# Kernel tuning notes

Measured on AMD Instinct MI355X. Metric: run time of the kernel, lower is better.

The kernel has to match this reference:

```python
import jax, jax.numpy as jnp
import numpy as np

N, T, C, H = 512, 64, 64, 4
HD = C // H
FE = 4  # forward_expansion
EPS = 1e-5


def _p(key, shape, scale=0.05):
    return jax.random.normal(key, shape, dtype=jnp.float32) * scale


def setup_inputs() -> dict:
    key = jax.random.key(0)
    ks = jax.random.split(key, 24)
    return {
        'value': jax.random.normal(ks[0], (N, T, C), dtype=jnp.float32),
        'key_t': jax.random.normal(ks[1], (N, T, C), dtype=jnp.float32),
        'query': jax.random.normal(ks[2], (N, T, C), dtype=jnp.float32),
        'adj': jax.random.uniform(ks[3], (N, N), dtype=jnp.float32),
        # SSelfAttention params (nn.Linear weights, applied as x @ W.T)
        'Wv': _p(ks[4], (HD, HD)), 'Wk': _p(ks[5], (HD, HD)), 'Wq': _p(ks[6], (HD, HD)),
        'Wo': _p(ks[7], (C, C)), 'bo': jnp.zeros((C,), jnp.float32),
        # LayerNorms
        'g1': jnp.ones((C,), jnp.float32), 'b1': jnp.zeros((C,), jnp.float32),
        'g2': jnp.ones((C,), jnp.float32), 'b2': jnp.zeros((C,), jnp.float32),
        # FFN
        'Wf1': _p(ks[8], (FE * C, C)), 'bf1': jnp.zeros((FE * C,), jnp.float32),
        'Wf2': _p(ks[9], (C, FE * C)), 'bf2': jnp.zeros((C,), jnp.float32),
        # GCN (two GraphConvolution layers: adj @ (x @ W) + b, ReLU between)
        'Wg1': _p(ks[10], (C, C)), 'bg1': jnp.zeros((C,), jnp.float32),
        'Wg2': _p(ks[11], (C, C)), 'bg2': jnp.zeros((C,), jnp.float32),
        # gating linears
        'Wo1': _p(ks[12], (C, C)), 'bo1': jnp.zeros((C,), jnp.float32),
        'Wo2': _p(ks[13], (C, C)), 'bo2': jnp.zeros((C,), jnp.float32),
    }


def _layernorm(x, g, b):
    m = jnp.mean(x, axis=-1, keepdims=True)
    v = jnp.mean((x - m) ** 2, axis=-1, keepdims=True)
    return (x - m) * jax.lax.rsqrt(v + EPS) * g + b


def reference(value, key_t, query, adj, Wv, Wk, Wq, Wo, bo, g1, b1, g2, b2,
              Wf1, bf1, Wf2, bf2, Wg1, bg1, Wg2, bg2, Wo1, bo1, Wo2, bo2):
    n, t, c = query.shape
    # --- SSelfAttention: attention across nodes (q/k axes are nodes) ---
    vh = value.reshape(n, t, H, HD) @ Wv.T
    kh = key_t.reshape(n, t, H, HD) @ Wk.T
    qh = query.reshape(n, t, H, HD) @ Wq.T
    energy = jnp.einsum('qthd,kthd->qkth', qh, kh)  # [N,N,T,H]
    att = jax.nn.softmax(energy / jnp.sqrt(jnp.float32(c)), axis=1)
    attn_out = jnp.einsum('qkth,kthd->qthd', att, vh).reshape(n, t, c)
    attn_out = attn_out @ Wo.T + bo
    # --- residual + norm + FFN + norm (dropout = identity, eval mode) ---
    x = _layernorm(attn_out + query, g1, b1)
    ffn = jax.nn.relu(x @ Wf1.T + bf1) @ Wf2.T + bf2
    out1 = _layernorm(ffn + x, g2, b2)
    # --- InstanceNorm2d(1) on adj: normalize over whole NxN map (no affine) ---
    am = jnp.mean(adj)
    av = jnp.mean((adj - am) ** 2)
    adj_n = (adj - am) * jax.lax.rsqrt(av + EPS)
    # --- GCN applied per-timestep, vectorized over T ---
    h = jax.nn.relu(jnp.einsum('nm,mtc->ntc', adj_n, query @ Wg1.T) + bg1)
    out2 = jnp.einsum('nm,mtc->ntc', adj_n, h @ Wg2.T) + bg2
    # --- gated fusion ---
    g = jax.nn.sigmoid(out1 @ Wo1.T + bo1 + out2 @ Wo2.T + bo2)
    return g * out1 + (1.0 - g) * out2
```

## Files before the change

kernel.cpp:

```cpp
#include <hip/hip_runtime.h>

#define LN_EPS 1e-5f

typedef __attribute__((ext_vector_type(4))) short short4v;
typedef __attribute__((ext_vector_type(4))) float float4v;

__device__ __forceinline__ float wave_sum(float v) {
#pragma unroll
  for (int o = 32; o > 0; o >>= 1) v += __shfl_xor(v, o, 64);
  return v;
}

__device__ __forceinline__ unsigned short f2b(float f) {
  unsigned int u = __float_as_uint(f);
  u += 0x7fffu + ((u >> 16) & 1u);
  return (unsigned short)(u >> 16);
}

__device__ __forceinline__ float b2f(unsigned short h) {
  return __uint_as_float(((unsigned int)h) << 16);
}

__device__ __forceinline__ float4v mfma_16x16x16_bf16(short4v a, short4v b,
                                                      float4v c) {
#if __has_builtin(__builtin_amdgcn_mfma_f32_16x16x16bf16_1k)
  return __builtin_amdgcn_mfma_f32_16x16x16bf16_1k(a, b, c, 0, 0, 0);
#else
  float4v d;
  asm volatile(
      "v_mfma_f32_16x16x16_bf16 %0, %1, %2, %3\n\ts_nop 7\n\ts_nop 7"
      : "=v"(d)
      : "v"(a), "v"(b), "v"(c));
  return d;
#endif
}

__global__ __launch_bounds__(256) void adj_part(const float* __restrict__ adj,
                                                float* __restrict__ ps,
                                                float* __restrict__ pss) {
  __shared__ float r1[4], r2[4];
  const int b = blockIdx.x, tid = threadIdx.x;
  float v0 = adj[b * 512 + tid], v1 = adj[b * 512 + 256 + tid];
  float s = v0 + v1;
  float ss = fmaf(v0, v0, v1 * v1);
  s = wave_sum(s);
  ss = wave_sum(ss);
  if ((tid & 63) == 0) { r1[tid >> 6] = s; r2[tid >> 6] = ss; }
  __syncthreads();
  if (tid == 0) {
    ps[b] = r1[0] + r1[1] + r1[2] + r1[3];
    pss[b] = r2[0] + r2[1] + r2[2] + r2[3];
  }
}

__global__ __launch_bounds__(256) void prep_kernel(
    const float* __restrict__ adj, const float* __restrict__ ps,
    const float* __restrict__ pss, const float* __restrict__ query,
    const float* __restrict__ Wg1, const float* __restrict__ Wf1,
    const float* __restrict__ Wf2, const float* __restrict__ Wo1,
    const float* __restrict__ Wo2, const float* __restrict__ Wg2,
    const float* __restrict__ bg2, const float* __restrict__ bo1,
    const float* __restrict__ bo2, unsigned short* __restrict__ anh,
    unsigned short* __restrict__ anl, unsigned short* __restrict__ Yfh,
    unsigned short* __restrict__ Yfl, unsigned short* __restrict__ Wf1f,
    unsigned short* __restrict__ Wf2f, unsigned short* __restrict__ Wo1f,
    unsigned short* __restrict__ Wg2hf, unsigned short* __restrict__ Wg2lf,
    unsigned short* __restrict__ W32hf, unsigned short* __restrict__ W32lf,
    float* __restrict__ c2) {
  __shared__ float r1[4], r2[4];
  __shared__ __align__(16) float pool[8320];
  const int tid = threadIdx.x, b = blockIdx.x;
  if (b < 256) {
    float s = ps[tid] + ps[tid + 256];
    float ss = pss[tid] + pss[tid + 256];
    s = wave_sum(s);
    ss = wave_sum(ss);
    if ((tid & 63) == 0) { r1[tid >> 6] = s; r2[tid >> 6] = ss; }
    __syncthreads();
    const float sum = r1[0] + r1[1] + r1[2] + r1[3];
    const float sqs = r2[0] + r2[1] + r2[2] + r2[3];
    const float am = sum * (1.f / 262144.f);
    const float var = sqs * (1.f / 262144.f) - am * am;
    const float rs = rsqrtf(var + LN_EPS);
    const int i = (b * 256 + tid) * 4;
    float4 v = *(const float4*)&adj[i];
    float vals[4] = {(v.x - am) * rs, (v.y - am) * rs, (v.z - am) * rs,
                     (v.w - am) * rs};
    unsigned short th[4], tl[4];
#pragma unroll
    for (int j = 0; j < 4; ++j) {
      th[j] = f2b(vals[j]);
      tl[j] = f2b(vals[j] - b2f(th[j]));
    }
    *(short4v*)&anh[i] = *(short4v*)th;
    *(short4v*)&anl[i] = *(short4v*)tl;
  } else if (b < 320) {
    const int id = (b - 256) * 256 + tid;
    const int n = id >> 6, k = id & 63;
    Wf1f[((k >> 4) * 256 + n) * 16 + (k & 15)] = f2b(Wf1[id]);
  } else if (b < 384) {
    const int id = (b - 320) * 256 + tid;
    const int n = id >> 8, k = id & 255;
    Wf2f[((k >> 4) * 64 + n) * 16 + (k & 15)] = f2b(Wf2[id]);
  } else if (b < 896) {
    const int pb = b - 384;
    const int w = tid >> 6, lane = tid & 63;
    const int mt = pb & 31;
    const int t = (pb >> 5) * 4 + w;
    float* xs = pool;
    float* Ls = pool + 256;
    float wc[64];
#pragma unroll
    for (int e = 0; e < 16; ++e)
      *(float4*)&wc[e * 4] = *(const float4*)&Wg1[lane * 64 + e * 4];
#pragma unroll 4
    for (int ms = 0; ms < 16; ++ms) {
      const int r = (mt * 16 + ms) * 64 + t;
      xs[w * 64 + lane] = query[r * 64 + lane];
      float acc = 0.f;
#pragma unroll
      for (int e = 0; e < 64; ++e) acc = fmaf(xs[w * 64 + e], wc[e], acc);
      Ls[(w * 16 + ms) * 68 + lane] = acc;
    }
    unsigned int dh[8], dl[8];
#pragma unroll
    for (int j = 0; j < 8; ++j) {
      float v0 = Ls[(w * 16 + 2 * j) * 68 + lane];
      float v1 = Ls[(w * 16 + 2 * j + 1) * 68 + lane];
      unsigned int h0 = f2b(v0), h1 = f2b(v1);
      unsigned int l0 = f2b(v0 - b2f((unsigned short)h0));
      unsigned int l1 = f2b(v1 - b2f((unsigned short)h1));
      dh[j] = h0 | (h1 << 16);
      dl[j] = l0 | (l1 << 16);
    }
    const int off = ((mt * 4096) + t * 64 + lane) * 16;
    *(uint4*)(Yfh + off) = *(uint4*)&dh[0];
    *(uint4*)(Yfh + off + 8) = *(uint4*)&dh[4];
    *(uint4*)(Yfl + off) = *(uint4*)&dl[0];
    *(uint4*)(Yfl + off + 8) = *(uint4*)&dl[4];
  } else if (b == 896) {
    for (int i = tid; i < 4096; i += 256) {
      const int n = i >> 6, k = i & 63;
      Wo1f[((k >> 4) * 64 + n) * 16 + (k & 15)] = f2b(Wo1[i]);
    }
  } else if (b == 897) {
    for (int i = tid; i < 4096; i += 256) {
      const int n = i >> 6, k = i & 63;
      const float v = Wg2[i];
      const unsigned short h = f2b(v);
      const unsigned short l = f2b(v - b2f(h));
      Wg2hf[((k >> 4) * 64 + n) * 16 + (k & 15)] = h;
      Wg2lf[((k >> 4) * 64 + n) * 16 + (k & 15)] = l;
    }
  } else {
    float* wo2s = pool;
    float* wg2s = pool + 4096;
    float* bg2s = pool + 8192;
    for (int i = tid; i < 4096; i += 256) {
      wo2s[i] = Wo2[i];
      wg2s[i] = Wg2[i];
    }
    if (tid < 64) bg2s[tid] = bg2[tid];
    __syncthreads();
#pragma unroll 4
    for (int t = 0; t < 16; ++t) {
      const int i = t * 256 + tid;
      const int r = i >> 6, c = i & 63;
      float acc = 0.f;
#pragma unroll
      for (int e = 0; e < 64; ++e)
        acc = fmaf(wo2s[r * 64 + e], wg2s[e * 64 + c], acc);
      const unsigned short h = f2b(acc);
      const unsigned short l = f2b(acc - b2f(h));
      W32hf[((c >> 4) * 64 + r) * 16 + (c & 15)] = h;
      W32lf[((c >> 4) * 64 + r) * 16 + (c & 15)] = l;
    }
    if (tid < 64) {
      float acc = bo1[tid] + bo2[tid];
#pragma unroll
      for (int e = 0; e < 64; ++e)
        acc = fmaf(wo2s[tid * 64 + e], bg2s[e], acc);
      c2[tid] = acc;
    }
  }
}

__global__ __launch_bounds__(512) void qkv2_kernel(
    const float* __restrict__ value, const float* __restrict__ keyt,
    const float* __restrict__ query, const float* __restrict__ Wv,
    const float* __restrict__ Wk, const float* __restrict__ Wq,
    unsigned short* __restrict__ vt, unsigned short* __restrict__ kh,
    unsigned short* __restrict__ qh) {
  __shared__ __align__(16) float wv[256], wk[256], wq[256];
  const int tid = threadIdx.x;
  if (tid < 256) {
    wv[tid] = Wv[tid];
    wk[tid] = Wk[tid];
    wq[tid] = Wq[tid] * 0.125f;
  }
  __syncthreads();
  const int th = blockIdx.x;
  const int t = th >> 2, h = th & 3;
  const int n = tid;
  const int base = t * 64 + h * 16;

  float y[16];
  unsigned short tmp[16];

#define XFORM(SRC, WARR)                                            \
  {                                                                 \
    const float4* p = (const float4*)(SRC + n * 4096 + base);       \
    float x[16];                                                    \
    *(float4*)(x + 0) = p[0];                                       \
    *(float4*)(x + 4) = p[1];                                       \
    *(float4*)(x + 8) = p[2];                                       \
    *(float4*)(x + 12) = p[3];                                      \
    _Pragma("unroll") for (int d = 0; d < 16; ++d) {                \
      float acc = 0.f;                                              \
      _Pragma("unroll") for (int e4 = 0; e4 < 4; ++e4) {            \
        float4 w4 = *(const float4*)&WARR[d * 16 + e4 * 4];         \
        acc = fmaf(w4.x, x[e4 * 4 + 0], acc);                       \
        acc = fmaf(w4.y, x[e4 * 4 + 1], acc);                       \
        acc = fmaf(w4.z, x[e4 * 4 + 2], acc);                       \
        acc = fmaf(w4.w, x[e4 * 4 + 3], acc);                       \
      }                                                             \
      y[d] = acc;                                                   \
    }                                                               \
  }

  XFORM(value, wv)
#pragma unroll
  for (int d = 0; d < 16; ++d) vt[th * 8192 + d * 512 + n] = f2b(y[d]);

  XFORM(keyt, wk)
#pragma unroll
  for (int d = 0; d < 16; ++d) tmp[d] = f2b(y[d]);
  *(int4*)&kh[(th * 512 + n) * 16] = *(int4*)&tmp[0];
  *(int4*)&kh[(th * 512 + n) * 16 + 8] = *(int4*)&tmp[8];

  XFORM(query, wq)
#pragma unroll
  for (int d = 0; d < 16; ++d) tmp[d] = f2b(y[d]);
  *(int4*)&qh[(th * 512 + n) * 16] = *(int4*)&tmp[0];
  *(int4*)&qh[(th * 512 + n) * 16 + 8] = *(int4*)&tmp[8];
#undef XFORM
}

#define VPAD 536
__global__ __launch_bounds__(256) void attn_mfma(
    const unsigned short* __restrict__ qh, const unsigned short* __restrict__ kh,
    const unsigned short* __restrict__ vt, float* __restrict__ o) {
  __shared__ __align__(16) unsigned short Vs[16 * VPAD];
  const int th = blockIdx.x >> 2;
  const int tid = threadIdx.x;
  {
    const unsigned short* vb = vt + th * 8192;
#pragma unroll
    for (int it = 0; it < 4; ++it) {
      const int flat = (it * 256 + tid) * 8;
      const int d = flat >> 9, k = flat & 511;
      *(int4*)&Vs[d * VPAD + k] = *(const int4*)&vb[flat];
    }
  }
  __syncthreads();

  const int lane = tid & 15;
  const int quad = (tid >> 4) & 3;
  const int w = tid >> 6;
  const int q0 = (blockIdx.x & 3) * 128 + w * 32;

  const unsigned short* qbase = qh + th * 8192;
  const unsigned short* kbase = kh + th * 8192;
  short4v qf[2];
#pragma unroll
  for (int ct = 0; ct < 2; ++ct)
    qf[ct] = *(const short4v*)&qbase[(q0 + ct * 16 + lane) * 16 + quad * 4];

  float4v acc[2];
  float l[2];
#pragma unroll
  for (int ct = 0; ct < 2; ++ct) {
    acc[ct].x = 0.f; acc[ct].y = 0.f; acc[ct].z = 0.f; acc[ct].w = 0.f;
    l[ct] = 0.f;
  }
  float4v zero;
  zero.x = 0.f; zero.y = 0.f; zero.z = 0.f; zero.w = 0.f;

  const unsigned short* vrow = &Vs[lane * VPAD];

  for (int kt = 0; kt < 32; ++kt) {
    const short4v kf =
        *(const short4v*)&kbase[(kt * 16 + lane) * 16 + quad * 4];
    const short4v vf = *(const short4v*)&vrow[kt * 16 + quad * 4];
#pragma unroll
    for (int ct = 0; ct < 2; ++ct) {
      float4v s = mfma_16x16x16_bf16(kf, qf[ct], zero);
      float p0 = __expf(s.x);
      float p1 = __expf(s.y);
      float p2 = __expf(s.z);
      float p3 = __expf(s.w);
      l[ct] += (p0 + p1) + (p2 + p3);
      unsigned int u0 = __float_as_uint(p0) + 0x8000u;
      unsigned int u1 = __float_as_uint(p1) + 0x8000u;
      unsigned int u2 = __float_as_uint(p2) + 0x8000u;
      unsigned int u3 = __float_as_uint(p3) + 0x8000u;
      union {
        uint2 u;
        short4v s4;
      } pk;
      pk.u.x = __builtin_amdgcn_perm(u1, u0, 0x07060302u);
      pk.u.y = __builtin_amdgcn_perm(u3, u2, 0x07060302u);
      acc[ct] = mfma_16x16x16_bf16(vf, pk.s4, acc[ct]);
    }
  }

#pragma unroll
  for (int ct = 0; ct < 2; ++ct) {
    float lt = l[ct];
    lt += __shfl_xor(lt, 16, 64);
    lt += __shfl_xor(lt, 32, 64);
    const float inv = 1.f / lt;
    float4 out;
    out.x = acc[ct].x * inv;
    out.y = acc[ct].y * inv;
    out.z = acc[ct].z * inv;
    out.w = acc[ct].w * inv;
    const int q = q0 + ct * 16 + lane;
    *(float4*)&o[th * 8192 + q * 16 + quad * 4] = out;
  }
}

__global__ __launch_bounds__(256) void xffn_fused(
    const float* __restrict__ o, const float* __restrict__ query,
    const float* __restrict__ Wo, const float* __restrict__ bo,
    const float* __restrict__ g1, const float* __restrict__ b1,
    const unsigned short* __restrict__ Wf1f, const float* __restrict__ bf1,
    const unsigned short* __restrict__ Wf2f, const float* __restrict__ bf2,
    const float* __restrict__ g2, const float* __restrict__ b2,
    float* __restrict__ out1, unsigned short* __restrict__ out1b) {
  __shared__ float xs_res[64][68];
  __shared__ __align__(16) unsigned short xb[64 * 68];
  __shared__ __align__(16) unsigned short hid[64 * 260];
  __shared__ float bcast[4][64];
  const int tid = threadIdx.x;
  const int w = tid >> 6, lane = tid & 63;
  const int ln = lane & 15, quad = lane >> 4;
  const int n = blockIdx.x;

  {
    float wc[64];
#pragma unroll
    for (int e = 0; e < 16; ++e)
      *(float4*)&wc[e * 4] = *(const float4*)&Wo[lane * 64 + e * 4];
    const float boc = bo[lane], gc = g1[lane], bc1 = b1[lane];
    const int hsel = lane >> 4, dsel = lane & 15;
    for (int i = 0; i < 16; ++i) {
      const int tt = w * 16 + i;
      bcast[w][lane] = o[(tt * 4 + hsel) * 8192 + n * 16 + dsel];
      float acc = 0.f;
#pragma unroll
      for (int e = 0; e < 64; ++e) acc = fmaf(bcast[w][e], wc[e], acc);
      float y = acc + boc + query[(n * 64 + tt) * 64 + lane];
      float mean = wave_sum(y) * 0.015625f;
      float d = y - mean;
      float var = wave_sum(d * d) * 0.015625f;
      float v = d * rsqrtf(var + LN_EPS) * gc + bc1;
      xs_res[tt][lane] = v;
      xb[tt * 68 + lane] = f2b(v);
    }
  }
  __syncthreads();

  {
    const int wm = (w & 1) * 32, wn = (w >> 1) * 128;
    float4v acc[2][8];
#pragma unroll
    for (int i = 0; i < 2; ++i)
#pragma unroll
      for (int j = 0; j < 8; ++j) {
        acc[i][j].x = 0.f; acc[i][j].y = 0.f;
        acc[i][j].z = 0.f; acc[i][j].w = 0.f;
      }
#pragma unroll
    for (int kt = 0; kt < 4; ++kt) {
      short4v a0 = *(const short4v*)&xb[(wm + ln) * 68 + kt * 16 + quad * 4];
      short4v a1 =
          *(const short4v*)&xb[(wm + 16 + ln) * 68 + kt * 16 + quad * 4];
#pragma unroll
      for (int j = 0; j < 8; ++j) {
        short4v bfr = *(const short4v*)&Wf1f[(kt * 256 + wn + j * 16 + ln) * 16 +
                                             quad * 4];
        acc[0][j] = mfma_16x16x16_bf16(a0, bfr, acc[0][j]);
        acc[1][j] = mfma_16x16x16_bf16(a1, bfr, acc[1][j]);
      }
    }
#pragma unroll
    for (int mt = 0; mt < 2; ++mt)
#pragma unroll
      for (int j = 0; j < 8; ++j) {
        const int col = wn + j * 16 + ln;
        const float bb = bf1[col];
#pragma unroll
        for (int reg = 0; reg < 4; ++reg) {
          const int row = wm + mt * 16 + quad * 4 + reg;
          hid[row * 260 + col] = f2b(fmaxf(acc[mt][j][reg] + bb, 0.f));
        }
      }
  }
  __syncthreads();

  {
    float4v acc[4];
#pragma unroll
    for (int j = 0; j < 4; ++j) {
      acc[j].x = 0.f; acc[j].y = 0.f; acc[j].z = 0.f; acc[j].w = 0.f;
    }
#pragma unroll 4
    for (int kt = 0; kt < 16; ++kt) {
      short4v a =
          *(const short4v*)&hid[(w * 16 + ln) * 260 + kt * 16 + quad * 4];
#pragma unroll
      for (int j = 0; j < 4; ++j) {
        short4v bfr =
            *(const short4v*)&Wf2f[(kt * 64 + j * 16 + ln) * 16 + quad * 4];
        acc[j] = mfma_16x16x16_bf16(a, bfr, acc[j]);
      }
    }
#pragma unroll
    for (int reg = 0; reg < 4; ++reg) {
      const int row = w * 16 + quad * 4 + reg;
      float v[4];
      float s = 0.f;
#pragma unroll
      for (int j = 0; j < 4; ++j) {
        v[j] = acc[j][reg] + bf2[j * 16 + ln] + xs_res[row][j * 16 + ln];
        s += v[j];
      }
      s += __shfl_xor(s, 1, 64);
      s += __shfl_xor(s, 2, 64);
      s += __shfl_xor(s, 4, 64);
      s += __shfl_xor(s, 8, 64);
      const float mean = s * 0.015625f;
      float vv = 0.f;
#pragma unroll
      for (int j = 0; j < 4; ++j) {
        const float dd = v[j] - mean;
        vv += dd * dd;
      }
      vv += __shfl_xor(vv, 1, 64);
      vv += __shfl_xor(vv, 2, 64);
      vv += __shfl_xor(vv, 4, 64);
      vv += __shfl_xor(vv, 8, 64);
      const float rs = rsqrtf(vv * 0.015625f + LN_EPS);
#pragma unroll
      for (int j = 0; j < 4; ++j) {
        const float ov = (v[j] - mean) * rs * g2[j * 16 + ln] + b2[j * 16 + ln];
        const int idx = (n * 64 + row) * 64 + j * 16 + ln;
        out1[idx] = ov;
        out1b[idx] = f2b(ov);
      }
    }
  }
}

__global__ __launch_bounds__(256) void gcn_gemm1(
    const unsigned short* __restrict__ Ah, const unsigned short* __restrict__ Al,
    const unsigned short* __restrict__ Bh, const unsigned short* __restrict__ Bl,
    const float* __restrict__ bg1, unsigned short* __restrict__ Hh,
    unsigned short* __restrict__ Hl) {
  const int tid = threadIdx.x;
  const int wave = tid >> 6, lane = tid & 63;
  const int ln = lane & 15, quad = lane >> 4;
  const int wm = (wave & 1) * 32, wn = (wave >> 1) * 64;
  const int m0 = blockIdx.y * 64 + wm;
  const int n0 = blockIdx.x * 128 + wn;

  const unsigned short* ah0 = Ah + (m0 + ln) * 512 + quad * 4;
  const unsigned short* al0 = Al + (m0 + ln) * 512 + quad * 4;
  const unsigned short* bh0 = Bh + (n0 + ln) * 16 + quad * 4;
  const unsigned short* bl0 = Bl + (n0 + ln) * 16 + quad * 4;

  float4v acc[2][4];
#pragma unroll
  for (int i = 0; i < 2; ++i)
#pragma unroll
    for (int j = 0; j < 4; ++j) {
      acc[i][j].x = 0.f; acc[i][j].y = 0.f;
      acc[i][j].z = 0.f; acc[i][j].w = 0.f;
    }

#pragma unroll 2
  for (int kt = 0; kt < 32; ++kt) {
    short4v a0h = *(const short4v*)(ah0 + kt * 16);
    short4v a1h = *(const short4v*)(ah0 + 16 * 512 + kt * 16);
    short4v a0l = *(const short4v*)(al0 + kt * 16);
    short4v a1l = *(const short4v*)(al0 + 16 * 512 + kt * 16);
#pragma unroll
    for (int j = 0; j < 4; ++j) {
      const int boff = (kt * 4096 + j * 16) * 16;
      short4v bh = *(const short4v*)(bh0 + boff);
      short4v bl = *(const short4v*)(bl0 + boff);
      acc[0][j] = mfma_16x16x16_bf16(a0l, bh, acc[0][j]);
      acc[0][j] = mfma_16x16x16_bf16(a0h, bl, acc[0][j]);
      acc[0][j] = mfma_16x16x16_bf16(a0h, bh, acc[0][j]);
      acc[1][j] = mfma_16x16x16_bf16(a1l, bh, acc[1][j]);
      acc[1][j] = mfma_16x16x16_bf16(a1h, bl, acc[1][j]);
      acc[1][j] = mfma_16x16x16_bf16(a1h, bh, acc[1][j]);
    }
  }

#pragma unroll
  for (int mt = 0; mt < 2; ++mt) {
    const int mtile = (m0 + mt * 16) >> 4;
#pragma unroll
    for (int j = 0; j < 4; ++j) {
      const int col = n0 + j * 16 + ln;
      const float bb = bg1[col & 63];
      unsigned short hh[4], hl[4];
#pragma unroll
      for (int reg = 0; reg < 4; ++reg) {
        float v = fmaxf(acc[mt][j][reg] + bb, 0.f);
        hh[reg] = f2b(v);
        hl[reg] = f2b(v - b2f(hh[reg]));
      }
      const int off = (mtile * 4096 + col) * 16 + quad * 4;
      *(uint2*)&Hh[off] = *(uint2*)hh;
      *(uint2*)&Hl[off] = *(uint2*)hl;
    }
  }
}

__global__ __launch_bounds__(256) void gcn_gemm2(
    const unsigned short* __restrict__ Ah, const unsigned short* __restrict__ Al,
    const unsigned short* __restrict__ Bh, const unsigned short* __restrict__ Bl,
    unsigned short* __restrict__ G2h, unsigned short* __restrict__ G2l) {
  const int tid = threadIdx.x;
  const int wave = tid >> 6, lane = tid & 63;
  const int ln = lane & 15, quad = lane >> 4;
  const int wm = (wave & 1) * 32, wn = (wave >> 1) * 64;
  const int m0 = blockIdx.y * 64 + wm;
  const int n0 = blockIdx.x * 128 + wn;

  const unsigned short* ah0 = Ah + (m0 + ln) * 512 + quad * 4;
  const unsigned short* al0 = Al + (m0 + ln) * 512 + quad * 4;
  const unsigned short* bh0 = Bh + (n0 + ln) * 16 + quad * 4;
  const unsigned short* bl0 = Bl + (n0 + ln) * 16 + quad * 4;

  float4v acc[2][4];
#pragma unroll
  for (int i = 0; i < 2; ++i)
#pragma unroll
    for (int j = 0; j < 4; ++j) {
      acc[i][j].x = 0.f; acc[i][j].y = 0.f;
      acc[i][j].z = 0.f; acc[i][j].w = 0.f;
    }

#pragma unroll 2
  for (int kt = 0; kt < 32; ++kt) {
    short4v a0h = *(const short4v*)(ah0 + kt * 16);
    short4v a1h = *(const short4v*)(ah0 + 16 * 512 + kt * 16);
    short4v a0l = *(const short4v*)(al0 + kt * 16);
    short4v a1l = *(const short4v*)(al0 + 16 * 512 + kt * 16);
#pragma unroll
    for (int j = 0; j < 4; ++j) {
      const int boff = (kt * 4096 + j * 16) * 16;
      short4v bh = *(const short4v*)(bh0 + boff);
      short4v bl = *(const short4v*)(bl0 + boff);
      acc[0][j] = mfma_16x16x16_bf16(a0l, bh, acc[0][j]);
      acc[0][j] = mfma_16x16x16_bf16(a0h, bl, acc[0][j]);
      acc[0][j] = mfma_16x16x16_bf16(a0h, bh, acc[0][j]);
      acc[1][j] = mfma_16x16x16_bf16(a1l, bh, acc[1][j]);
      acc[1][j] = mfma_16x16x16_bf16(a1h, bl, acc[1][j]);
      acc[1][j] = mfma_16x16x16_bf16(a1h, bh, acc[1][j]);
    }
  }

#pragma unroll
  for (int mt = 0; mt < 2; ++mt)
#pragma unroll
    for (int j = 0; j < 4; ++j) {
      const int col = n0 + j * 16 + ln;
#pragma unroll
      for (int reg = 0; reg < 4; ++reg) {
        const int row = m0 + mt * 16 + quad * 4 + reg;
        const float v = acc[mt][j][reg];
        const unsigned short h = f2b(v);
        G2h[row * 4096 + col] = h;
        G2l[row * 4096 + col] = f2b(v - b2f(h));
      }
    }
}

__global__ __launch_bounds__(256) void gate_mfma(
    const unsigned short* __restrict__ out1b, const float* __restrict__ out1,
    const unsigned short* __restrict__ G2h, const unsigned short* __restrict__ G2l,
    const unsigned short* __restrict__ Wo1f, const unsigned short* __restrict__ Wg2hf,
    const unsigned short* __restrict__ Wg2lf, const unsigned short* __restrict__ W32hf,
    const unsigned short* __restrict__ W32lf, const float* __restrict__ bg2,
    const float* __restrict__ c2, float* __restrict__ dst) {
  const int tid = threadIdx.x;
  const int wave = tid >> 6, lane = tid & 63;
  const int ln = lane & 15, quad = lane >> 4;
  const int m0 = blockIdx.x * 64 + wave * 16;

  const unsigned short* o1p = out1b + (m0 + ln) * 64 + quad * 4;
  const unsigned short* ghp = G2h + (m0 + ln) * 64 + quad * 4;
  const unsigned short* glp = G2l + (m0 + ln) * 64 + quad * 4;

  float4v aco[4], aca[4];
#pragma unroll
  for (int j = 0; j < 4; ++j) {
    aco[j].x = 0.f; aco[j].y = 0.f; aco[j].z = 0.f; aco[j].w = 0.f;
    aca[j].x = 0.f; aca[j].y = 0.f; aca[j].z = 0.f; aca[j].w = 0.f;
  }

#pragma unroll
  for (int kt = 0; kt < 4; ++kt) {
    const short4v ao = *(const short4v*)(o1p + kt * 16);
    const short4v gh = *(const short4v*)(ghp + kt * 16);
    const short4v gl = *(const short4v*)(glp + kt * 16);
#pragma unroll
    for (int j = 0; j < 4; ++j) {
      const int boff = (kt * 64 + j * 16 + ln) * 16 + quad * 4;
      const short4v wgh = *(const short4v*)(Wg2hf + boff);
      const short4v wgl = *(const short4v*)(Wg2lf + boff);
      const short4v wo1 = *(const short4v*)(Wo1f + boff);
      const short4v w3h = *(const short4v*)(W32hf + boff);
      const short4v w3l = *(const short4v*)(W32lf + boff);
      aco[j] = mfma_16x16x16_bf16(gl, wgh, aco[j]);
      aco[j] = mfma_16x16x16_bf16(gh, wgl, aco[j]);
      aco[j] = mfma_16x16x16_bf16(gh, wgh, aco[j]);
      aca[j] = mfma_16x16x16_bf16(ao, wo1, aca[j]);
      aca[j] = mfma_16x16x16_bf16(gl, w3h, aca[j]);
      aca[j] = mfma_16x16x16_bf16(gh, w3l, aca[j]);
      aca[j] = mfma_16x16x16_bf16(gh, w3h, aca[j]);
    }
  }

#pragma unroll
  for (int j = 0; j < 4; ++j) {
    const int col = j * 16 + ln;
    const float bg2v = bg2[col];
    const float c2v = c2[col];
#pragma unroll
    for (int reg = 0; reg < 4; ++reg) {
      const int row = m0 + quad * 4 + reg;
      const float o2 = aco[j][reg] + bg2v;
      const float a = aca[j][reg] + c2v;
      const float o1v = out1[row * 64 + col];
      const float g = 1.f / (1.f + __expf(-a));
      dst[row * 64 + col] = o2 + g * (o1v - o2);
    }
  }
}

extern "C" void kernel_launch(void* const* d_in, const int* in_sizes, int n_in,
                              void* d_out, int out_size, void* d_ws,
                              size_t ws_size, hipStream_t stream) {
  const float* value = (const float*)d_in[0];
  const float* key_t = (const float*)d_in[1];
  const float* query = (const float*)d_in[2];
  const float* adj = (const float*)d_in[3];
  const float* Wv = (const float*)d_in[4];
  const float* Wk = (const float*)d_in[5];
  const float* Wq = (const float*)d_in[6];
  const float* Wo = (const float*)d_in[7];
  const float* bo = (const float*)d_in[8];
  const float* g1 = (const float*)d_in[9];
  const float* b1 = (const float*)d_in[10];
  const float* g2 = (const float*)d_in[11];
  const float* b2 = (const float*)d_in[12];
  const float* Wf1 = (const float*)d_in[13];
  const float* bf1 = (const float*)d_in[14];
  const float* Wf2 = (const float*)d_in[15];
  const float* bf2 = (const float*)d_in[16];
  const float* Wg1 = (const float*)d_in[17];
  const float* bg1 = (const float*)d_in[18];
  const float* Wg2 = (const float*)d_in[19];
  const float* bg2 = (const float*)d_in[20];
  const float* Wo1 = (const float*)d_in[21];
  const float* bo1 = (const float*)d_in[22];
  const float* Wo2 = (const float*)d_in[23];
  const float* bo2 = (const float*)d_in[24];

  float* ws = (float*)d_ws;
  const size_t M1 = 1048576;
  float* o = ws + 0;
  float* out1 = ws + 2 * M1;
  unsigned short* out1b = (unsigned short*)(ws + 4 * M1);
  unsigned short* qh = (unsigned short*)(ws + 5 * M1);
  unsigned short* kh = (unsigned short*)(ws + 6 * M1);
  unsigned short* vt = (unsigned short*)(ws + 7 * M1);
  unsigned short* Yfh = (unsigned short*)(ws + 8 * M1);
  unsigned short* Yfl = (unsigned short*)(ws + 9 * M1);
  unsigned short* Hrfh = (unsigned short*)(ws + 10 * M1);
  unsigned short* Hrfl = (unsigned short*)(ws + 11 * M1);
  unsigned short* G2h = (unsigned short*)(ws + 12 * M1);
  unsigned short* G2l = (unsigned short*)(ws + 13 * M1);
  unsigned short* anh = (unsigned short*)(ws + 14 * M1);
  unsigned short* anl = (unsigned short*)(ws + 14 * M1 + 131072);
  float* wbase = ws + 14 * M1 + 262144;
  unsigned short* Wf1f = (unsigned short*)(wbase);
  unsigned short* Wf2f = (unsigned short*)(wbase + 8192);
  unsigned short* Wo1f = (unsigned short*)(wbase + 16384);
  unsigned short* Wg2hf = (unsigned short*)(wbase + 18432);
  unsigned short* Wg2lf = (unsigned short*)(wbase + 20480);
  unsigned short* W32hf = (unsigned short*)(wbase + 22528);
  unsigned short* W32lf = (unsigned short*)(wbase + 24576);
  float* c2 = wbase + 26624;
  float* ps = wbase + 26688;
  float* pss = ps + 512;
  float* dst = (float*)d_out;

  adj_part<<<512, 256, 0, stream>>>(adj, ps, pss);
  prep_kernel<<<899, 256, 0, stream>>>(adj, ps, pss, query, Wg1, Wf1, Wf2,
                                       Wo1, Wo2, Wg2, bg2, bo1, bo2, anh, anl,
                                       Yfh, Yfl, Wf1f, Wf2f, Wo1f, Wg2hf,
                                       Wg2lf, W32hf, W32lf, c2);
  qkv2_kernel<<<256, 512, 0, stream>>>(value, key_t, query, Wv, Wk, Wq, vt, kh, qh);
  attn_mfma<<<1024, 256, 0, stream>>>(qh, kh, vt, o);
  xffn_fused<<<512, 256, 0, stream>>>(o, query, Wo, bo, g1, b1, Wf1f, bf1,
                                      Wf2f, bf2, g2, b2, out1, out1b);
  gcn_gemm1<<<dim3(32, 8), 256, 0, stream>>>(anh, anl, Yfh, Yfl, bg1, Hrfh,
                                             Hrfl);
  gcn_gemm2<<<dim3(32, 8), 256, 0, stream>>>(anh, anl, Hrfh, Hrfl, G2h, G2l);
  gate_mfma<<<512, 256, 0, stream>>>(out1b, out1, G2h, G2l, Wo1f, Wg2hf,
                                     Wg2lf, W32hf, W32lf, bg2, c2, dst);
}
```

Baseline: 268.5 us.

## Merge independent stages into fewer launches via block-index dispatch

Merges the eight kernel launches into five. Each new kernel branches on block index so that independent work runs side by side: adj partial sums with the QKV projection, prep work with attention, and the FFN with GCN gemm1. The second GCN gemm is retiled to 64x64 blocks, giving 512 blocks instead of 256 for more parallelism. This removes launch gaps and lets small stages fill idle compute units, at the cost of larger shared memory per block and mixed block types with different register needs.

```diff
diff --git a/kernel.cpp b/kernel.cpp
--- a/kernel.cpp
+++ b/kernel.cpp
@@ -35,177 +35,38 @@
 #endif
 }
 
-__global__ __launch_bounds__(256) void adj_part(const float* __restrict__ adj,
-                                                float* __restrict__ ps,
-                                                float* __restrict__ pss) {
+__global__ __launch_bounds__(256) void s1_kernel(
+    const float* __restrict__ adj, float* __restrict__ ps,
+    float* __restrict__ pss, const float* __restrict__ value,
+    const float* __restrict__ keyt, const float* __restrict__ query,
+    const float* __restrict__ Wv, const float* __restrict__ Wk,
+    const float* __restrict__ Wq, unsigned short* __restrict__ vt,
+    unsigned short* __restrict__ kh, unsigned short* __restrict__ qh) {
   __shared__ float r1[4], r2[4];
+  __shared__ __align__(16) float wv[256], wk[256], wq[256];
   const int b = blockIdx.x, tid = threadIdx.x;
-  float v0 = adj[b * 512 + tid], v1 = adj[b * 512 + 256 + tid];
-  float s = v0 + v1;
-  float ss = fmaf(v0, v0, v1 * v1);
-  s = wave_sum(s);
-  ss = wave_sum(ss);
-  if ((tid & 63) == 0) { r1[tid >> 6] = s; r2[tid >> 6] = ss; }
-  __syncthreads();
-  if (tid == 0) {
-    ps[b] = r1[0] + r1[1] + r1[2] + r1[3];
-    pss[b] = r2[0] + r2[1] + r2[2] + r2[3];
-  }
-}
-
-__global__ __launch_bounds__(256) void prep_kernel(
-    const float* __restrict__ adj, const float* __restrict__ ps,
-    const float* __restrict__ pss, const float* __restrict__ query,
-    const float* __restrict__ Wg1, const float* __restrict__ Wf1,
-    const float* __restrict__ Wf2, const float* __restrict__ Wo1,
-    const float* __restrict__ Wo2, const float* __restrict__ Wg2,
-    const float* __restrict__ bg2, const float* __restrict__ bo1,
-    const float* __restrict__ bo2, unsigned short* __restrict__ anh,
-    unsigned short* __restrict__ anl, unsigned short* __restrict__ Yfh,
-    unsigned short* __restrict__ Yfl, unsigned short* __restrict__ Wf1f,
-    unsigned short* __restrict__ Wf2f, unsigned short* __restrict__ Wo1f,
-    unsigned short* __restrict__ Wg2hf, unsigned short* __restrict__ Wg2lf,
-    unsigned short* __restrict__ W32hf, unsigned short* __restrict__ W32lf,
-    float* __restrict__ c2) {
-  __shared__ float r1[4], r2[4];
-  __shared__ __align__(16) float pool[8320];
-  const int tid = threadIdx.x, b = blockIdx.x;
-  if (b < 256) {
-    float s = ps[tid] + ps[tid + 256];
-    float ss = pss[tid] + pss[tid + 256];
+  if (b < 512) {
+    float v0 = adj[b * 512 + tid], v1 = adj[b * 512 + 256 + tid];
+    float s = v0 + v1;
+    float ss = fmaf(v0, v0, v1 * v1);
     s = wave_sum(s);
     ss = wave_sum(ss);
     if ((tid & 63) == 0) { r1[tid >> 6] = s; r2[tid >> 6] = ss; }
     __syncthreads();
-    const float sum = r1[0] + r1[1] + r1[2] + r1[3];
-    const float sqs = r2[0] + r2[1] + r2[2] + r2[3];
-    const float am = sum * (1.f / 262144.f);
-    const float var = sqs * (1.f / 262144.f) - am * am;
-    const float rs = rsqrtf(var + LN_EPS);
-    const int i = (b * 256 + tid) * 4;
-    float4 v = *(const float4*)&adj[i];
-    float vals[4] = {(v.x - am) * rs, (v.y - am) * rs, (v.z - am) * rs,
-                     (v.w - am) * rs};
-    unsigned short th[4], tl[4];
-#pragma unroll
-    for (int j = 0; j < 4; ++j) {
-      th[j] = f2b(vals[j]);
-      tl[j] = f2b(vals[j] - b2f(th[j]));
-    }
-    *(short4v*)&anh[i] = *(short4v*)th;
-    *(short4v*)&anl[i] = *(short4v*)tl;
-  } else if (b < 320) {
-    const int id = (b - 256) * 256 + tid;
-    const int n = id >> 6, k = id & 63;
-    Wf1f[((k >> 4) * 256 + n) * 16 + (k & 15)] = f2b(Wf1[id]);
-  } else if (b < 384) {
-    const int id = (b - 320) * 256 + tid;
-    const int n = id >> 8, k = id & 255;
-    Wf2f[((k >> 4) * 64 + n) * 16 + (k & 15)] = f2b(Wf2[id]);
-  } else if (b < 896) {
-    const int pb = b - 384;
-    const int w = tid >> 6, lane = tid & 63;
-    const int mt = pb & 31;
-    const int t = (pb >> 5) * 4 + w;
-    float* xs = pool;
-    float* Ls = pool + 256;
-    float wc[64];
-#pragma unroll
-    for (int e = 0; e < 16; ++e)
-      *(float4*)&wc[e * 4] = *(const float4*)&Wg1[lane * 64 + e * 4];
-#pragma unroll 4
-    for (int ms = 0; ms < 16; ++ms) {
-      const int r = (mt * 16 + ms) * 64 + t;
-      xs[w * 64 + lane] = query[r * 64 + lane];
-      float acc = 0.f;
-#pragma unroll
-      for (int e = 0; e < 64; ++e) acc = fmaf(xs[w * 64 + e], wc[e], acc);
-      Ls[(w * 16 + ms) * 68 + lane] = acc;
-    }
-    unsigned int dh[8], dl[8];
-#pragma unroll
-    for (int j = 0; j < 8; ++j) {
-      float v0 = Ls[(w * 16 + 2 * j) * 68 + lane];
-      float v1 = Ls[(w * 16 + 2 * j + 1) * 68 + lane];
-      unsigned int h0 = f2b(v0), h1 = f2b(v1);
-      unsigned int l0 = f2b(v0 - b2f((unsigned short)h0));
-      unsigned int l1 = f2b(v1 - b2f((unsigned short)h1));
-      dh[j] = h0 | (h1 << 16);
-      dl[j] = l0 | (l1 << 16);
-    }
-    const int off = ((mt * 4096) + t * 64 + lane) * 16;
-    *(uint4*)(Yfh + off) = *(uint4*)&dh[0];
-    *(uint4*)(Yfh + off + 8) = *(uint4*)&dh[4];
-    *(uint4*)(Yfl + off) = *(uint4*)&dl[0];
-    *(uint4*)(Yfl + off + 8) = *(uint4*)&dl[4];
-  } else if (b == 896) {
-    for (int i = tid; i < 4096; i += 256) {
-      const int n = i >> 6, k = i & 63;
-      Wo1f[((k >> 4) * 64 + n) * 16 + (k & 15)] = f2b(Wo1[i]);
-    }
-  } else if (b == 897) {
-    for (int i = tid; i < 4096; i += 256) {
-      const int n = i >> 6, k = i & 63;
-      const float v = Wg2[i];
-      const unsigned short h = f2b(v);
-      const unsigned short l = f2b(v - b2f(h));
-      Wg2hf[((k >> 4) * 64 + n) * 16 + (k & 15)] = h;
-      Wg2lf[((k >> 4) * 64 + n) * 16 + (k & 15)] = l;
+    if (tid == 0) {
+      ps[b] = r1[0] + r1[1] + r1[2] + r1[3];
+      pss[b] = r2[0] + r2[1] + r2[2] + r2[3];
     }
   } else {
-    float* wo2s = pool;
-    float* wg2s = pool + 4096;
-    float* bg2s = pool + 8192;
-    for (int i = tid; i < 4096; i += 256) {
-      wo2s[i] = Wo2[i];
-      wg2s[i] = Wg2[i];
-    }
-    if (tid < 64) bg2s[tid] = bg2[tid];
-    __syncthreads();
-#pragma unroll 4
-    for (int t = 0; t < 16; ++t) {
-      const int i = t * 256 + tid;
-      const int r = i >> 6, c = i & 63;
-      float acc = 0.f;
-#pragma unroll
-      for (int e = 0; e < 64; ++e)
-        acc = fmaf(wo2s[r * 64 + e], wg2s[e * 64 + c], acc);
-      const unsigned short h = f2b(acc);
-      const unsigned short l = f2b(acc - b2f(h));
-      W32hf[((c >> 4) * 64 + r) * 16 + (c & 15)] = h;
-      W32lf[((c >> 4) * 64 + r) * 16 + (c & 15)] = l;
-    }
-    if (tid < 64) {
-      float acc = bo1[tid] + bo2[tid];
-#pragma unroll
-      for (int e = 0; e < 64; ++e)
-        acc = fmaf(wo2s[tid * 64 + e], bg2s[e], acc);
-      c2[tid] = acc;
-    }
-  }
-}
-
-__global__ __launch_bounds__(512) void qkv2_kernel(
-    const float* __restrict__ value, const float* __restrict__ keyt,
-    const float* __restrict__ query, const float* __restrict__ Wv,
-    const float* __restrict__ Wk, const float* __restrict__ Wq,
-    unsigned short* __restrict__ vt, unsigned short* __restrict__ kh,
-    unsigned short* __restrict__ qh) {
-  __shared__ __align__(16) float wv[256], wk[256], wq[256];
-  const int tid = threadIdx.x;
-  if (tid < 256) {
     wv[tid] = Wv[tid];
     wk[tid] = Wk[tid];
     wq[tid] = Wq[tid] * 0.125f;
-  }
-  __syncthreads();
-  const int th = blockIdx.x;
-  const int t = th >> 2, h = th & 3;
-  const int n = tid;
-  const int base = t * 64 + h * 16;
-
-  float y[16];
-  unsigned short tmp[16];
+    __syncthreads();
+    const int th = b - 512;
+    const int t = th >> 2, h = th & 3;
+    const int base = t * 64 + h * 16;
+    float y[16];
+    unsigned short tmp[16];
 
 #define XFORM(SRC, WARR)                                            \
   {                                                                 \
@@ -228,275 +89,476 @@
     }                                                               \
   }
 
-  XFORM(value, wv)
-#pragma unroll
-  for (int d = 0; d < 16; ++d) vt[th * 8192 + d * 512 + n] = f2b(y[d]);
-
-  XFORM(keyt, wk)
-#pragma unroll
-  for (int d = 0; d < 16; ++d) tmp[d] = f2b(y[d]);
-  *(int4*)&kh[(th * 512 + n) * 16] = *(int4*)&tmp[0];
-  *(int4*)&kh[(th * 512 + n) * 16 + 8] = *(int4*)&tmp[8];
-
-  XFORM(query, wq)
-#pragma unroll
-  for (int d = 0; d < 16; ++d) tmp[d] = f2b(y[d]);
-  *(int4*)&qh[(th * 512 + n) * 16] = *(int4*)&tmp[0];
-  *(int4*)&qh[(th * 512 + n) * 16 + 8] = *(int4*)&tmp[8];
+    for (int s = 0; s < 2; ++s) {
+      const int n = tid + (s << 8);
+      XFORM(value, wv)
+#pragma unroll
+      for (int d = 0; d < 16; ++d) vt[th * 8192 + d * 512 + n] = f2b(y[d]);
+      XFORM(keyt, wk)
+#pragma unroll
+      for (int d = 0; d < 16; ++d) tmp[d] = f2b(y[d]);
+      *(int4*)&kh[(th * 512 + n) * 16] = *(int4*)&tmp[0];
+      *(int4*)&kh[(th * 512 + n) * 16 + 8] = *(int4*)&tmp[8];
+      XFORM(query, wq)
+#pragma unroll
+      for (int d = 0; d < 16; ++d) tmp[d] = f2b(y[d]);
+      *(int4*)&qh[(th * 512 + n) * 16] = *(int4*)&tmp[0];
+      *(int4*)&qh[(th * 512 + n) * 16 + 8] = *(int4*)&tmp[8];
+    }
 #undef XFORM
+  }
 }
 
 #define VPAD 536
-__global__ __launch_bounds__(256) void attn_mfma(
-    const unsigned short* __restrict__ qh, const unsigned short* __restrict__ kh,
-    const unsigned short* __restrict__ vt, float* __restrict__ o) {
-  __shared__ __align__(16) unsigned short Vs[16 * VPAD];
-  const int th = blockIdx.x >> 2;
-  const int tid = threadIdx.x;
-  {
-    const unsigned short* vb = vt + th * 8192;
-#pragma unroll
-    for (int it = 0; it < 4; ++it) {
-      const int flat = (it * 256 + tid) * 8;
-      const int d = flat >> 9, k = flat & 511;
-      *(int4*)&Vs[d * VPAD + k] = *(const int4*)&vb[flat];
+__global__ __launch_bounds__(256) void s2_kernel(
+    const float* __restrict__ adj, const float* __restrict__ ps,
+    const float* __restrict__ pss, const float* __restrict__ query,
+    const float* __restrict__ Wg1, const float* __restrict__ Wf1,
+    const float* __restrict__ Wf2, const float* __restrict__ Wo1,
+    const float* __restrict__ Wo2, const float* __restrict__ Wg2,
+    const float* __restrict__ bg2, const float* __restrict__ bo1,
+    const float* __restrict__ bo2, unsigned short* __restrict__ anh,
+    unsigned short* __restrict__ anl, unsigned short* __restrict__ Yfh,
+    unsigned short* __restrict__ Yfl, unsigned short* __restrict__ Wf1f,
+    unsigned short* __restrict__ Wf2f, unsigned short* __restrict__ Wo1f,
+    unsigned short* __restrict__ Wg2hf, unsigned short* __restrict__ Wg2lf,
+    unsigned short* __restrict__ W32hf, unsigned short* __restrict__ W32lf,
+    float* __restrict__ c2, const unsigned short* __restrict__ qh,
+    const unsigned short* __restrict__ kh, const unsigned short* __restrict__ vt,
+    float* __restrict__ o) {
+  __shared__ float r1[4], r2[4];
+  __shared__ __align__(16) char smem[33280];
+  const int tid = threadIdx.x, b = blockIdx.x;
+  if (b < 899) {
+    float* pool = (float*)smem;
+    if (b < 256) {
+      float s = ps[tid] + ps[tid + 256];
+      float ss = pss[tid] + pss[tid + 256];
+      s = wave_sum(s);
+      ss = wave_sum(ss);
+      if ((tid & 63) == 0) { r1[tid >> 6] = s; r2[tid >> 6] = ss; }
+      __syncthreads();
+      const float sum = r1[0] + r1[1] + r1[2] + r1[3];
+      const float sqs = r2[0] + r2[1] + r2[2] + r2[3];
+      const float am = sum * (1.f / 262144.f);
+      const float var = sqs * (1.f / 262144.f) - am * am;
+      const float rs = rsqrtf(var + LN_EPS);
+      const int i = (b * 256 + tid) * 4;
+      float4 v = *(const float4*)&adj[i];
+      float vals[4] = {(v.x - am) * rs, (v.y - am) * rs, (v.z - am) * rs,
+                       (v.w - am) * rs};
+      unsigned short th4[4], tl4[4];
+#pragma unroll
+      for (int j = 0; j < 4; ++j) {
+        th4[j] = f2b(vals[j]);
+        tl4[j] = f2b(vals[j] - b2f(th4[j]));
+      }
+      *(short4v*)&anh[i] = *(short4v*)th4;
+      *(short4v*)&anl[i] = *(short4v*)tl4;
+    } else if (b < 320) {
+      const int id = (b - 256) * 256 + tid;
+      const int n = id >> 6, k = id & 63;
+      Wf1f[((k >> 4) * 256 + n) * 16 + (k & 15)] = f2b(Wf1[id]);
+    } else if (b < 384) {
+      const int id = (b - 320) * 256 + tid;
+      const int n = id >> 8, k = id & 255;
+      Wf2f[((k >> 4) * 64 + n) * 16 + (k & 15)] = f2b(Wf2[id]);
+    } else if (b < 896) {
+      const int pb = b - 384;
+      const int w = tid >> 6, lane = tid & 63;
+      const int mt = pb & 31;
+      const int t = (pb >> 5) * 4 + w;
+      float* xs = pool;
+      float* Ls = pool + 256;
+      float wc[64];
+#pragma unroll
+      for (int e = 0; e < 16; ++e)
+        *(float4*)&wc[e * 4] = *(const float4*)&Wg1[lane * 64 + e * 4];
+#pragma unroll 4
+      for (int ms = 0; ms < 16; ++ms) {
+        const int r = (mt * 16 + ms) * 64 + t;
+        xs[w * 64 + lane] = query[r * 64 + lane];
+        float acc = 0.f;
+#pragma unroll
+        for (int e = 0; e < 64; ++e) acc = fmaf(xs[w * 64 + e], wc[e], acc);
+        Ls[(w * 16 + ms) * 68 + lane] = acc;
+      }
+      unsigned int dh[8], dl[8];
+#pragma unroll
+      for (int j = 0; j < 8; ++j) {
+        float v0 = Ls[(w * 16 + 2 * j) * 68 + lane];
+        float v1 = Ls[(w * 16 + 2 * j + 1) * 68 + lane];
+        unsigned int h0 = f2b(v0), h1 = f2b(v1);
+        unsigned int l0 = f2b(v0 - b2f((unsigned short)h0));
+        unsigned int l1 = f2b(v1 - b2f((unsigned short)h1));
+        dh[j] = h0 | (h1 << 16);
+        dl[j] = l0 | (l1 << 16);
+      }
+      const int off = ((mt * 4096) + t * 64 + lane) * 16;
+      *(uint4*)(Yfh + off) = *(uint4*)&dh[0];
+      *(uint4*)(Yfh + off + 8) = *(uint4*)&dh[4];
+      *(uint4*)(Yfl + off) = *(uint4*)&dl[0];
+      *(uint4*)(Yfl + off + 8) = *(uint4*)&dl[4];
+    } else if (b == 896) {
+      for (int i = tid; i < 4096; i += 256) {
+        const int n = i >> 6, k = i & 63;
+        Wo1f[((k >> 4) * 64 + n) * 16 + (k & 15)] = f2b(Wo1[i]);
+      }
+    } else if (b == 897) {
+      for (int i = tid; i < 4096; i += 256) {
+        const int n = i >> 6, k = i & 63;
+        const float v = Wg2[i];
+        const unsigned short h = f2b(v);
+        const unsigned short l = f2b(v - b2f(h));
+        Wg2hf[((k >> 4) * 64 + n) * 16 + (k & 15)] = h;
+        Wg2lf[((k >> 4) * 64 + n) * 16 + (k & 15)] = l;
+      }
+    } else {
+      float* wo2s = pool;
+      float* wg2s = pool + 4096;
+      float* bg2s = pool + 8192;
+      for (int i = tid; i < 4096; i += 256) {
+        wo2s[i] = Wo2[i];
+        wg2s[i] = Wg2[i];
+      }
+      if (tid < 64) bg2s[tid] = bg2[tid];
+      __syncthreads();
+#pragma unroll 4
+      for (int t = 0; t < 16; ++t) {
+        const int i = t * 256 + tid;
+        const int r = i >> 6, c = i & 63;
+        float acc = 0.f;
+#pragma unroll
+        for (int e = 0; e < 64; ++e)
+          acc = fmaf(wo2s[r * 64 + e], wg2s[e * 64 + c], acc);
+        const unsigned short h = f2b(acc);
+        const unsigned short l = f2b(acc - b2f(h));
+        W32hf[((c >> 4) * 64 + r) * 16 + (c & 15)] = h;
+        W32lf[((c >> 4) * 64 + r) * 16 + (c & 15)] = l;
+      }
+      if (tid < 64) {
+        float acc = bo1[tid] + bo2[tid];
+#pragma unroll
+        for (int e = 0; e < 64; ++e)
+          acc = fmaf(wo2s[tid * 64 + e], bg2s[e], acc);
+        c2[tid] = acc;
+      }
+    }
+  } else {
+    unsigned short* Vs = (unsigned short*)smem;
+    const int bx = b - 899;
+    const int th = bx >> 2;
+    {
+      const unsigned short* vb = vt + th * 8192;
+#pragma unroll
+      for (int it = 0; it < 4; ++it) {
+        const int flat = (it * 256 + tid) * 8;
+        const int d = flat >> 9, k = flat & 511;
+        *(int4*)&Vs[d * VPAD + k] = *(const int4*)&vb[flat];
+      }
+    }
+    __syncthreads();
+
+    const int lane = tid & 15;
+    const int quad = (tid >> 4) & 3;
+    const int w = tid >> 6;
+    const int q0 = (bx & 3) * 128 + w * 32;
+
+    const unsigned short* qbase = qh + th * 8192;
+    const unsigned short* kbase = kh + th * 8192;
+    short4v qf[2];
+#pragma unroll
+    for (int ct = 0; ct < 2; ++ct)
+      qf[ct] = *(const short4v*)&qbase[(q0 + ct * 16 + lane) * 16 + quad * 4];
+
+    float4v acc[2];
+    float l[2];
+#pragma unroll
+    for (int ct = 0; ct < 2; ++ct) {
+      acc[ct].x = 0.f; acc[ct].y = 0.f; acc[ct].z = 0.f; acc[ct].w = 0.f;
+      l[ct] = 0.f;
+    }
+    float4v zero;
+    zero.x = 0.f; zero.y = 0.f; zero.z = 0.f; zero.w = 0.f;
+
+    const unsigned short* vrow = &Vs[lane * VPAD];
+
+    for (int kt = 0; kt < 32; ++kt) {
+      const short4v kf =
+          *(const short4v*)&kbase[(kt * 16 + lane) * 16 + quad * 4];
+      const short4v vf = *(const short4v*)&vrow[kt * 16 + quad * 4];
+#pragma unroll
+      for (int ct = 0; ct < 2; ++ct) {
+        float4v s = mfma_16x16x16_bf16(kf, qf[ct], zero);
+        float p0 = __expf(s.x);
+        float p1 = __expf(s.y);
+        float p2 = __expf(s.z);
+        float p3 = __expf(s.w);
+        l[ct] += (p0 + p1) + (p2 + p3);
+        unsigned int u0 = __float_as_uint(p0) + 0x8000u;
+        unsigned int u1 = __float_as_uint(p1) + 0x8000u;
+        unsigned int u2 = __float_as_uint(p2) + 0x8000u;
+        unsigned int u3 = __float_as_uint(p3) + 0x8000u;
+        union {
+          uint2 u;
+          short4v s4;
+        } pk;
+        pk.u.x = __builtin_amdgcn_perm(u1, u0, 0x07060302u);
+        pk.u.y = __builtin_amdgcn_perm(u3, u2, 0x07060302u);
+        acc[ct] = mfma_16x16x16_bf16(vf, pk.s4, acc[ct]);
+      }
+    }
+
+#pragma unroll
+    for (int ct = 0; ct < 2; ++ct) {
+      float lt = l[ct];
+      lt += __shfl_xor(lt, 16, 64);
+      lt += __shfl_xor(lt, 32, 64);
+      const float inv = 1.f / lt;
+      float4 out;
+      out.x = acc[ct].x * inv;
+      out.y = acc[ct].y * inv;
+      out.z = acc[ct].z * inv;
+      out.w = acc[ct].w * inv;
+      const int q = q0 + ct * 16 + lane;
+      *(float4*)&o[th * 8192 + q * 16 + quad * 4] = out;
     }
   }
-  __syncthreads();
-
-  const int lane = tid & 15;
-  const int quad = (tid >> 4) & 3;
-  const int w = tid >> 6;
-  const int q0 = (blockIdx.x & 3) * 128 + w * 32;
-
-  const unsigned short* qbase = qh + th * 8192;
-  const unsigned short* kbase = kh + th * 8192;
-  short4v qf[2];
-#pragma unroll
-  for (int ct = 0; ct < 2; ++ct)
-    qf[ct] = *(const short4v*)&qbase[(q0 + ct * 16 + lane) * 16 + quad * 4];
-
-  float4v acc[2];
-  float l[2];
-#pragma unroll
-  for (int ct = 0; ct < 2; ++ct) {
-    acc[ct].x = 0.f; acc[ct].y = 0.f; acc[ct].z = 0.f; acc[ct].w = 0.f;
-    l[ct] = 0.f;
-  }
-  float4v zero;
-  zero.x = 0.f; zero.y = 0.f; zero.z = 0.f; zero.w = 0.f;
-
-  const unsigned short* vrow = &Vs[lane * VPAD];
-
-  for (int kt = 0; kt < 32; ++kt) {
-    const short4v kf =
-        *(const short4v*)&kbase[(kt * 16 + lane) * 16 + quad * 4];
-    const short4v vf = *(const short4v*)&vrow[kt * 16 + quad * 4];
-#pragma unroll
-    for (int ct = 0; ct < 2; ++ct) {
-      float4v s = mfma_16x16x16_bf16(kf, qf[ct], zero);
-      float p0 = __expf(s.x);
-      float p1 = __expf(s.y);
-      float p2 = __expf(s.z);
-      float p3 = __expf(s.w);
-      l[ct] += (p0 + p1) + (p2 + p3);
-      unsigned int u0 = __float_as_uint(p0) + 0x8000u;
-      unsigned int u1 = __float_as_uint(p1) + 0x8000u;
-      unsigned int u2 = __float_as_uint(p2) + 0x8000u;
-      unsigned int u3 = __float_as_uint(p3) + 0x8000u;
-      union {
-        uint2 u;
-        short4v s4;
-      } pk;
-      pk.u.x = __builtin_amdgcn_perm(u1, u0, 0x07060302u);
-      pk.u.y = __builtin_amdgcn_perm(u3, u2, 0x07060302u);
-      acc[ct] = mfma_16x16x16_bf16(vf, pk.s4, acc[ct]);
-    }
-  }
-
-#pragma unroll
-  for (int ct = 0; ct < 2; ++ct) {
-    float lt = l[ct];
-    lt += __shfl_xor(lt, 16, 64);
-    lt += __shfl_xor(lt, 32, 64);
-    const float inv = 1.f / lt;
-    float4 out;
-    out.x = acc[ct].x * inv;
-    out.y = acc[ct].y * inv;
-    out.z = acc[ct].z * inv;
-    out.w = acc[ct].w * inv;
-    const int q = q0 + ct * 16 + lane;
-    *(float4*)&o[th * 8192 + q * 16 + quad * 4] = out;
-  }
-}
-
-__global__ __launch_bounds__(256) void xffn_fused(
+}
+
+__global__ __launch_bounds__(256) void s3_kernel(
     const float* __restrict__ o, const float* __restrict__ query,
     const float* __restrict__ Wo, const float* __restrict__ bo,
     const float* __restrict__ g1, const float* __restrict__ b1,
     const unsigned short* __restrict__ Wf1f, const float* __restrict__ bf1,
     const unsigned short* __restrict__ Wf2f, const float* __restrict__ bf2,
     const float* __restrict__ g2, const float* __restrict__ b2,
-    float* __restrict__ out1, unsigned short* __restrict__ out1b) {
-  __shared__ float xs_res[64][68];
-  __shared__ __align__(16) unsigned short xb[64 * 68];
-  __shared__ __align__(16) unsigned short hid[64 * 260];
-  __shared__ float bcast[4][64];
-  const int tid = threadIdx.x;
-  const int w = tid >> 6, lane = tid & 63;
-  const int ln = lane & 15, quad = lane >> 4;
-  const int n = blockIdx.x;
-
-  {
-    float wc[64];
-#pragma unroll
-    for (int e = 0; e < 16; ++e)
-      *(float4*)&wc[e * 4] = *(const float4*)&Wo[lane * 64 + e * 4];
-    const float boc = bo[lane], gc = g1[lane], bc1 = b1[lane];
-    const int hsel = lane >> 4, dsel = lane & 15;
-    for (int i = 0; i < 16; ++i) {
-      const int tt = w * 16 + i;
-      bcast[w][lane] = o[(tt * 4 + hsel) * 8192 + n * 16 + dsel];
-      float acc = 0.f;
-#pragma unroll
-      for (int e = 0; e < 64; ++e) acc = fmaf(bcast[w][e], wc[e], acc);
-      float y = acc + boc + query[(n * 64 + tt) * 64 + lane];
-      float mean = wave_sum(y) * 0.015625f;
-      float d = y - mean;
-      float var = wave_sum(d * d) * 0.015625f;
-      float v = d * rsqrtf(var + LN_EPS) * gc + bc1;
-      xs_res[tt][lane] = v;
-      xb[tt * 68 + lane] = f2b(v);
-    }
-  }
-  __syncthreads();
-
-  {
-    const int wm = (w & 1) * 32, wn = (w >> 1) * 128;
-    float4v acc[2][8];
-#pragma unroll
-    for (int i = 0; i < 2; ++i)
-#pragma unroll
-      for (int j = 0; j < 8; ++j) {
-        acc[i][j].x = 0.f; acc[i][j].y = 0.f;
-        acc[i][j].z = 0.f; acc[i][j].w = 0.f;
-      }
-#pragma unroll
-    for (int kt = 0; kt < 4; ++kt) {
-      short4v a0 = *(const short4v*)&xb[(wm + ln) * 68 + kt * 16 + quad * 4];
-      short4v a1 =
-          *(const short4v*)&xb[(wm + 16 + ln) * 68 + kt * 16 + quad * 4];
-#pragma unroll
-      for (int j = 0; j < 8; ++j) {
-        short4v bfr = *(const short4v*)&Wf1f[(kt * 256 + wn + j * 16 + ln) * 16 +
-                                             quad * 4];
-        acc[0][j] = mfma_16x16x16_bf16(a0, bfr, acc[0][j]);
-        acc[1][j] = mfma_16x16x16_bf16(a1, bfr, acc[1][j]);
-      }
-    }
-#pragma unroll
-    for (int mt = 0; mt < 2; ++mt)
-#pragma unroll
-      for (int j = 0; j < 8; ++j) {
-        const int col = wn + j * 16 + ln;
-        const float bb = bf1[col];
-#pragma unroll
-        for (int reg = 0; reg < 4; ++reg) {
-          const int row = wm + mt * 16 + quad * 4 + reg;
-          hid[row * 260 + col] = f2b(fmaxf(acc[mt][j][reg] + bb, 0.f));
-        }
-      }
-  }
-  __syncthreads();
-
-  {
-    float4v acc[4];
-#pragma unroll
-    for (int j = 0; j < 4; ++j) {
-      acc[j].x = 0.f; acc[j].y = 0.f; acc[j].z = 0.f; acc[j].w = 0.f;
-    }
-#pragma unroll 4
-    for (int kt = 0; kt < 16; ++kt) {
-      short4v a =
-          *(const short4v*)&hid[(w * 16 + ln) * 260 + kt * 16 + quad * 4];
-#pragma unroll
-      for (int j = 0; j < 4; ++j) {
-        short4v bfr =
-            *(const short4v*)&Wf2f[(kt * 64 + j * 16 + ln) * 16 + quad * 4];
-        acc[j] = mfma_16x16x16_bf16(a, bfr, acc[j]);
-      }
-    }
-#pragma unroll
-    for (int reg = 0; reg < 4; ++reg) {
-      const int row = w * 16 + quad * 4 + reg;
-      float v[4];
-      float s = 0.f;
-#pragma unroll
-      for (int j = 0; j < 4; ++j) {
-        v[j] = acc[j][reg] + bf2[j * 16 + ln] + xs_res[row][j * 16 + ln];
-        s += v[j];
-      }
-      s += __shfl_xor(s, 1, 64);
-      s += __shfl_xor(s, 2, 64);
-      s += __shfl_xor(s, 4, 64);
-      s += __shfl_xor(s, 8, 64);
-      const float mean = s * 0.015625f;
-      float vv = 0.f;
-#pragma unroll
-      for (int j = 0; j < 4; ++j) {
-        const float dd = v[j] - mean;
-        vv += dd * dd;
-      }
-      vv += __shfl_xor(vv, 1, 64);
-      vv += __shfl_xor(vv, 2, 64);
-      vv += __shfl_xor(vv, 4, 64);
-      vv += __shfl_xor(vv, 8, 64);
-      const float rs = rsqrtf(vv * 0.015625f + LN_EPS);
-#pragma unroll
-      for (int j = 0; j < 4; ++j) {
-        const float ov = (v[j] - mean) * rs * g2[j * 16 + ln] + b2[j * 16 + ln];
-        const int idx = (n * 64 + row) * 64 + j * 16 + ln;
-        out1[idx] = ov;
-        out1b[idx] = f2b(ov);
-      }
-    }
-  }
-}
-
-__global__ __launch_bounds__(256) void gcn_gemm1(
+    float* __restrict__ out1, unsigned short* __restrict__ out1b,
     const unsigned short* __restrict__ Ah, const unsigned short* __restrict__ Al,
     const unsigned short* __restrict__ Bh, const unsigned short* __restrict__ Bl,
     const float* __restrict__ bg1, unsigned short* __restrict__ Hh,
     unsigned short* __restrict__ Hl) {
+  __shared__ __align__(16) char smem[60416];
+  const int tid = threadIdx.x, b = blockIdx.x;
+  const int w = tid >> 6, lane = tid & 63;
+  const int ln = lane & 15, quad = lane >> 4;
+  if (b < 512) {
+    float* xs_res = (float*)smem;
+    unsigned short* xb = (unsigned short*)(smem + 17408);
+    unsigned short* hid = (unsigned short*)(smem + 26112);
+    float* bcast = (float*)(smem + 59392);
+    const int n = b;
+    {
+      float wc[64];
+#pragma unroll
+      for (int e = 0; e < 16; ++e)
+        *(float4*)&wc[e * 4] = *(const float4*)&Wo[lane * 64 + e * 4];
+      const float boc = bo[lane], gc = g1[lane], bc1 = b1[lane];
+      const int hsel = lane >> 4, dsel = lane & 15;
+      for (int i = 0; i < 16; ++i) {
+        const int tt = w * 16 + i;
+        bcast[w * 64 + lane] = o[(tt * 4 + hsel) * 8192 + n * 16 + dsel];
+        float acc = 0.f;
+#pragma unroll
+        for (int e = 0; e < 64; ++e) acc = fmaf(bcast[w * 64 + e], wc[e], acc);
+        float y = acc + boc + query[(n * 64 + tt) * 64 + lane];
+        float mean = wave_sum(y) * 0.015625f;
+        float d = y - mean;
+        float var = wave_sum(d * d) * 0.015625f;
+        float v = d * rsqrtf(var + LN_EPS) * gc + bc1;
+        xs_res[tt * 68 + lane] = v;
+        xb[tt * 68 + lane] = f2b(v);
+      }
+    }
+    __syncthreads();
+
+    {
+      const int wm = (w & 1) * 32, wn = (w >> 1) * 128;
+      float4v acc[2][8];
+#pragma unroll
+      for (int i = 0; i < 2; ++i)
+#pragma unroll
+        for (int j = 0; j < 8; ++j) {
+          acc[i][j].x = 0.f; acc[i][j].y = 0.f;
+          acc[i][j].z = 0.f; acc[i][j].w = 0.f;
+        }
+#pragma unroll
+      for (int kt = 0; kt < 4; ++kt) {
+        short4v a0 = *(const short4v*)&xb[(wm + ln) * 68 + kt * 16 + quad * 4];
+        short4v a1 =
+            *(const short4v*)&xb[(wm + 16 + ln) * 68 + kt * 16 + quad * 4];
+#pragma unroll
+        for (int j = 0; j < 8; ++j) {
+          short4v bfr = *(const short4v*)&Wf1f[(kt * 256 + wn + j * 16 + ln) *
+                                                   16 + quad * 4];
+          acc[0][j] = mfma_16x16x16_bf16(a0, bfr, acc[0][j]);
+          acc[1][j] = mfma_16x16x16_bf16(a1, bfr, acc[1][j]);
+        }
+      }
+#pragma unroll
+      for (int mt = 0; mt < 2; ++mt)
+#pragma unroll
+        for (int j = 0; j < 8; ++j) {
+          const int col = wn + j * 16 + ln;
+          const float bb = bf1[col];
+#pragma unroll
+          for (int reg = 0; reg < 4; ++reg) {
+            const int row = wm + mt * 16 + quad * 4 + reg;
+            hid[row * 260 + col] = f2b(fmaxf(acc[mt][j][reg] + bb, 0.f));
+          }
+        }
+    }
+    __syncthreads();
+
+    {
+      float4v acc[4];
+#pragma unroll
+      for (int j = 0; j < 4; ++j) {
+        acc[j].x = 0.f; acc[j].y = 0.f; acc[j].z = 0.f; acc[j].w = 0.f;
+      }
+#pragma unroll 4
+      for (int kt = 0; kt < 16; ++kt) {
+        short4v a =
+            *(const short4v*)&hid[(w * 16 + ln) * 260 + kt * 16 + quad * 4];
+#pragma unroll
+        for (int j = 0; j < 4; ++j) {
+          short4v bfr =
+              *(const short4v*)&Wf2f[(kt * 64 + j * 16 + ln) * 16 + quad * 4];
+          acc[j] = mfma_16x16x16_bf16(a, bfr, acc[j]);
+        }
+      }
+#pragma unroll
+      for (int reg = 0; reg < 4; ++reg) {
+        const int row = w * 16 + quad * 4 + reg;
+        float v[4];
+        float s = 0.f;
+#pragma unroll
+        for (int j = 0; j < 4; ++j) {
+          v[j] = acc[j][reg] + bf2[j * 16 + ln] + xs_res[row * 68 + j * 16 + ln];
+          s += v[j];
+        }
+        s += __shfl_xor(s, 1, 64);
+        s += __shfl_xor(s, 2, 64);
+        s += __shfl_xor(s, 4, 64);
+        s += __shfl_xor(s, 8, 64);
+        const float mean = s * 0.015625f;
+        float vv = 0.f;
+#pragma unroll
+        for (int j = 0; j < 4; ++j) {
+          const float dd = v[j] - mean;
+          vv += dd * dd;
+        }
+        vv += __shfl_xor(vv, 1, 64);
+        vv += __shfl_xor(vv, 2, 64);
+        vv += __shfl_xor(vv, 4, 64);
+        vv += __shfl_xor(vv, 8, 64);
+        const float rs = rsqrtf(vv * 0.015625f + LN_EPS);
+#pragma unroll
+        for (int j = 0; j < 4; ++j) {
+          const float ov =
+              (v[j] - mean) * rs * g2[j * 16 + ln] + b2[j * 16 + ln];
+          const int idx = (n * 64 + row) * 64 + j * 16 + ln;
+          out1[idx] = ov;
+          out1b[idx] = f2b(ov);
+        }
+      }
+    }
+  } else {
+    const int pb = b - 512;
+    const int wave = w;
+    const int wm = (wave & 1) * 32, wn = (wave >> 1) * 64;
+    const int m0 = (pb >> 5) * 64 + wm;
+    const int n0 = (pb & 31) * 128 + wn;
+
+    const unsigned short* ah0 = Ah + (m0 + ln) * 512 + quad * 4;
+    const unsigned short* al0 = Al + (m0 + ln) * 512 + quad * 4;
+    const unsigned short* bh0 = Bh + (n0 + ln) * 16 + quad * 4;
+    const unsigned short* bl0 = Bl + (n0 + ln) * 16 + quad * 4;
+
+    float4v acc[2][4];
+#pragma unroll
+    for (int i = 0; i < 2; ++i)
+#pragma unroll
+      for (int j = 0; j < 4; ++j) {
+        acc[i][j].x = 0.f; acc[i][j].y = 0.f;
+        acc[i][j].z = 0.f; acc[i][j].w = 0.f;
+      }
+
+#pragma unroll 2
+    for (int kt = 0; kt < 32; ++kt) {
+      short4v a0h = *(const short4v*)(ah0 + kt * 16);
+      short4v a1h = *(const short4v*)(ah0 + 16 * 512 + kt * 16);
+      short4v a0l = *(const short4v*)(al0 + kt * 16);
+      short4v a1l = *(const short4v*)(al0 + 16 * 512 + kt * 16);
+#pragma unroll
+      for (int j = 0; j < 4; ++j) {
+        const int boff = (kt * 4096 + j * 16) * 16;
+        short4v bh = *(const short4v*)(bh0 + boff);
+        short4v bl = *(const short4v*)(bl0 + boff);
+        acc[0][j] = mfma_16x16x16_bf16(a0l, bh, acc[0][j]);
+        acc[0][j] = mfma_16x16x16_bf16(a0h, bl, acc[0][j]);
+        acc[0][j] = mfma_16x16x16_bf16(a0h, bh, acc[0][j]);
+        acc[1][j] = mfma_16x16x16_bf16(a1l, bh, acc[1][j]);
+        acc[1][j] = mfma_16x16x16_bf16(a1h, bl, acc[1][j]);
+        acc[1][j] = mfma_16x16x16_bf16(a1h, bh, acc[1][j]);
+      }
+    }
+
+#pragma unroll
+    for (int mt = 0; mt < 2; ++mt) {
+      const int mtile = (m0 + mt * 16) >> 4;
+#pragma unroll
+      for (int j = 0; j < 4; ++j) {
+        const int col = n0 + j * 16 + ln;
+        const float bb = bg1[col & 63];
+        unsigned short hh[4], hl[4];
+#pragma unroll
+        for (int reg = 0; reg < 4; ++reg) {
+          float v = fmaxf(acc[mt][j][reg] + bb, 0.f);
+          hh[reg] = f2b(v);
+          hl[reg] = f2b(v - b2f(hh[reg]));
+        }
+        const int off = (mtile * 4096 + col) * 16 + quad * 4;
+        *(uint2*)&Hh[off] = *(uint2*)hh;
+        *(uint2*)&Hl[off] = *(uint2*)hl;
+      }
+    }
+  }
+}
+
+__global__ __launch_bounds__(256) void s4_kernel(
+    const unsigned short* __restrict__ Ah, const unsigned short* __restrict__ Al,
+    const unsigned short* __restrict__ Bh, const unsigned short* __restrict__ Bl,
+    unsigned short* __restrict__ G2h, unsigned short* __restrict__ G2l) {
   const int tid = threadIdx.x;
   const int wave = tid >> 6, lane = tid & 63;
   const int ln = lane & 15, quad = lane >> 4;
-  const int wm = (wave & 1) * 32, wn = (wave >> 1) * 64;
-  const int m0 = blockIdx.y * 64 + wm;
-  const int n0 = blockIdx.x * 128 + wn;
+  const int wm = (wave & 1) * 32, wn = (wave >> 1) * 32;
+  const int m0 = (blockIdx.x >> 6) * 64 + wm;
+  const int n0 = (blockIdx.x & 63) * 64 + wn;
 
   const unsigned short* ah0 = Ah + (m0 + ln) * 512 + quad * 4;
   const unsigned short* al0 = Al + (m0 + ln) * 512 + quad * 4;
   const unsigned short* bh0 = Bh + (n0 + ln) * 16 + quad * 4;
   const unsigned short* bl0 = Bl + (n0 + ln) * 16 + quad * 4;
 
-  float4v acc[2][4];
+  float4v acc[2][2];
 #pragma unroll
   for (int i = 0; i < 2; ++i)
 #pragma unroll
-    for (int j = 0; j < 4; ++j) {
+    for (int j = 0; j < 2; ++j) {
       acc[i][j].x = 0.f; acc[i][j].y = 0.f;
       acc[i][j].z = 0.f; acc[i][j].w = 0.f;
     }
 
-#pragma unroll 2
+#pragma unroll 4
   for (int kt = 0; kt < 32; ++kt) {
     short4v a0h = *(const short4v*)(ah0 + kt * 16);
     short4v a1h = *(const short4v*)(ah0 + 16 * 512 + kt * 16);
     short4v a0l = *(const short4v*)(al0 + kt * 16);
     short4v a1l = *(const short4v*)(al0 + 16 * 512 + kt * 16);
 #pragma unroll
-    for (int j = 0; j < 4; ++j) {
+    for (int j = 0; j < 2; ++j) {
       const int boff = (kt * 4096 + j * 16) * 16;
       short4v bh = *(const short4v*)(bh0 + boff);
       short4v bl = *(const short4v*)(bl0 + boff);
@@ -510,75 +572,9 @@
   }
 
 #pragma unroll
-  for (int mt = 0; mt < 2; ++mt) {
-    const int mtile = (m0 + mt * 16) >> 4;
-#pragma unroll
-    for (int j = 0; j < 4; ++j) {
-      const int col = n0 + j * 16 + ln;
-      const float bb = bg1[col & 63];
-      unsigned short hh[4], hl[4];
-#pragma unroll
-      for (int reg = 0; reg < 4; ++reg) {
-        float v = fmaxf(acc[mt][j][reg] + bb, 0.f);
-        hh[reg] = f2b(v);
-        hl[reg] = f2b(v - b2f(hh[reg]));
-      }
-      const int off = (mtile * 4096 + col) * 16 + quad * 4;
-      *(uint2*)&Hh[off] = *(uint2*)hh;
-      *(uint2*)&Hl[off] = *(uint2*)hl;
-    }
-  }
-}
-
-__global__ __launch_bounds__(256) void gcn_gemm2(
-    const unsigned short* __restrict__ Ah, const unsigned short* __restrict__ Al,
-    const unsigned short* __restrict__ Bh, const unsigned short* __restrict__ Bl,
-    unsigned short* __restrict__ G2h, unsigned short* __restrict__ G2l) {
-  const int tid = threadIdx.x;
-  const int wave = tid >> 6, lane = tid & 63;
-  const int ln = lane & 15, quad = lane >> 4;
-  const int wm = (wave & 1) * 32, wn = (wave >> 1) * 64;
-  const int m0 = blockIdx.y * 64 + wm;
-  const int n0 = blockIdx.x * 128 + wn;
-
-  const unsigned short* ah0 = Ah + (m0 + ln) * 512 + quad * 4;
-  const unsigned short* al0 = Al + (m0 + ln) * 512 + quad * 4;
-  const unsigned short* bh0 = Bh + (n0 + ln) * 16 + quad * 4;
-  const unsigned short* bl0 = Bl + (n0 + ln) * 16 + quad * 4;
-
-  float4v acc[2][4];
-#pragma unroll
-  for (int i = 0; i < 2; ++i)
-#pragma unroll
-    for (int j = 0; j < 4; ++j) {
-      acc[i][j].x = 0.f; acc[i][j].y = 0.f;
-      acc[i][j].z = 0.f; acc[i][j].w = 0.f;
-    }
-
-#pragma unroll 2
-  for (int kt = 0; kt < 32; ++kt) {
-    short4v a0h = *(const short4v*)(ah0 + kt * 16);
-    short4v a1h = *(const short4v*)(ah0 + 16 * 512 + kt * 16);
-    short4v a0l = *(const short4v*)(al0 + kt * 16);
-    short4v a1l = *(const short4v*)(al0 + 16 * 512 + kt * 16);
-#pragma unroll
-    for (int j = 0; j < 4; ++j) {
-      const int boff = (kt * 4096 + j * 16) * 16;
-      short4v bh = *(const short4v*)(bh0 + boff);
-      short4v bl = *(const short4v*)(bl0 + boff);
-      acc[0][j] = mfma_16x16x16_bf16(a0l, bh, acc[0][j]);
-      acc[0][j] = mfma_16x16x16_bf16(a0h, bl, acc[0][j]);
-      acc[0][j] = mfma_16x16x16_bf16(a0h, bh, acc[0][j]);
-      acc[1][j] = mfma_16x16x16_bf16(a1l, bh, acc[1][j]);
-      acc[1][j] = mfma_16x16x16_bf16(a1h, bl, acc[1][j]);
-      acc[1][j] = mfma_16x16x16_bf16(a1h, bh, acc[1][j]);
-    }
-  }
-
-#pragma unroll
   for (int mt = 0; mt < 2; ++mt)
 #pragma unroll
-    for (int j = 0; j < 4; ++j) {
+    for (int j = 0; j < 2; ++j) {
       const int col = n0 + j * 16 + ln;
 #pragma unroll
       for (int reg = 0; reg < 4; ++reg) {
@@ -591,7 +587,7 @@
     }
 }
 
-__global__ __launch_bounds__(256) void gate_mfma(
+__global__ __launch_bounds__(256) void s5_kernel(
     const unsigned short* __restrict__ out1b, const float* __restrict__ out1,
     const unsigned short* __restrict__ G2h, const unsigned short* __restrict__ G2l,
     const unsigned short* __restrict__ Wo1f, const unsigned short* __restrict__ Wg2hf,
@@ -712,18 +708,16 @@
   float* pss = ps + 512;
   float* dst = (float*)d_out;
 
-  adj_part<<<512, 256, 0, stream>>>(adj, ps, pss);
-  prep_kernel<<<899, 256, 0, stream>>>(adj, ps, pss, query, Wg1, Wf1, Wf2,
-                                       Wo1, Wo2, Wg2, bg2, bo1, bo2, anh, anl,
-                                       Yfh, Yfl, Wf1f, Wf2f, Wo1f, Wg2hf,
-                                       Wg2lf, W32hf, W32lf, c2);
-  qkv2_kernel<<<256, 512, 0, stream>>>(value, key_t, query, Wv, Wk, Wq, vt, kh, qh);
-  attn_mfma<<<1024, 256, 0, stream>>>(qh, kh, vt, o);
-  xffn_fused<<<512, 256, 0, stream>>>(o, query, Wo, bo, g1, b1, Wf1f, bf1,
-                                      Wf2f, bf2, g2, b2, out1, out1b);
-  gcn_gemm1<<<dim3(32, 8), 256, 0, stream>>>(anh, anl, Yfh, Yfl, bg1, Hrfh,
-                                             Hrfl);
-  gcn_gemm2<<<dim3(32, 8), 256, 0, stream>>>(anh, anl, Hrfh, Hrfl, G2h, G2l);
-  gate_mfma<<<512, 256, 0, stream>>>(out1b, out1, G2h, G2l, Wo1f, Wg2hf,
+  s1_kernel<<<768, 256, 0, stream>>>(adj, ps, pss, value, key_t, query, Wv,
+                                     Wk, Wq, vt, kh, qh);
+  s2_kernel<<<1923, 256, 0, stream>>>(adj, ps, pss, query, Wg1, Wf1, Wf2, Wo1,
+                                      Wo2, Wg2, bg2, bo1, bo2, anh, anl, Yfh,
+                                      Yfl, Wf1f, Wf2f, Wo1f, Wg2hf, Wg2lf,
+                                      W32hf, W32lf, c2, qh, kh, vt, o);
+  s3_kernel<<<768, 256, 0, stream>>>(o, query, Wo, bo, g1, b1, Wf1f, bf1,
+                                     Wf2f, bf2, g2, b2, out1, out1b, anh, anl,
+                                     Yfh, Yfl, bg1, Hrfh, Hrfl);
+  s4_kernel<<<512, 256, 0, stream>>>(anh, anl, Hrfh, Hrfl, G2h, G2l);
+  s5_kernel<<<512, 256, 0, stream>>>(out1b, out1, G2h, G2l, Wo1f, Wg2hf,
                                      Wg2lf, W32hf, W32lf, bg2, c2, dst);
 }
```

New measurement: 277.1 us. +3.2%, slower.
